# Kernel tuning notes

Hardware: AMD Instinct MI355X
Metric: run time of the kernel (lower is better)

The kernel has to match this reference:

```python
import jax, jax.numpy as jnp
import numpy as np

NUM_ITERATIONS = 3

def squash(t, axis=-1):
    sq = jnp.clip(jnp.sum(t * t, axis=axis, keepdims=True), 1e-8, 1e4)
    norm = jnp.sqrt(sq)
    scale = sq / (1.0 + sq)
    return scale * (t / (norm + 1e-8))

def setup_inputs() -> dict:
    key = jax.random.key(0)
    k1, k2 = jax.random.split(key)
    B, N_in, N_out, D_in, D_out = 128, 1152, 10, 8, 16
    u = jax.random.normal(k1, (B, N_in, D_in), dtype=jnp.float32)
    W = jax.random.normal(k2, (N_in, N_out, D_out, D_in), dtype=jnp.float32) * 0.005
    return {"u": u, "W": W}

def reference(u, W):
    # u: [B, N_in, D_in]; W: [N_in, N_out, D_out, D_in]
    # u_hat: [B, N_in, N_out, D_out]
    u_hat = jnp.einsum('iodk,bik->biod', W, u)
    u_hat = jnp.clip(u_hat, -10.0, 10.0)
    B, N_in, N_out, _ = u_hat.shape
    b = jnp.zeros((B, N_in, N_out), dtype=u_hat.dtype)
    v = None
    for it in range(NUM_ITERATIONS):
        c = jax.nn.softmax(b, axis=2)                      # [B, N_in, N_out]
        s = jnp.einsum('bio,biod->bod', c, u_hat)          # [B, N_out, D_out]
        v = squash(s, axis=-1)                             # [B, N_out, D_out]
        if it < NUM_ITERATIONS - 1:
            agreement = jnp.einsum('biod,bod->bio', u_hat, v)
            b = b + jnp.clip(agreement, -10.0, 10.0)
    return v
```

## Files before the change

### kernel.cpp

```cpp
#include <hip/hip_runtime.h>
#include <cstddef>

#define NB    128
#define NIN   1152
#define NOUT  10
#define DOUT  16
#define OD    160
#define NSEG  36
#define SEGI  32
#define PGRID (NB / 2 * NSEG)

typedef __attribute__((ext_vector_type(4))) unsigned int u32x4;

#if __has_builtin(__builtin_amdgcn_fdot2_f32_bf16)
#define HAS_DOT2 1
typedef __attribute__((ext_vector_type(2))) __bf16 bf16x2;
__device__ __forceinline__ float dot2bf(unsigned w, unsigned uu, float c) {
    return __builtin_amdgcn_fdot2_f32_bf16(
        __builtin_bit_cast(bf16x2, w), __builtin_bit_cast(bf16x2, uu), c, false);
}
#else
#define HAS_DOT2 0
#endif

__device__ __forceinline__ unsigned short f2bf(float x) {
    union { float f; unsigned u; } v; v.f = x;
    const unsigned r = v.u + 0x7fffu + ((v.u >> 16) & 1u);
    return (unsigned short)(r >> 16);
}
__device__ __forceinline__ unsigned pack2(float a, float b) {
    return (unsigned)f2bf(a) | ((unsigned)f2bf(b) << 16);
}
__device__ __forceinline__ float lo2f(unsigned w) {
    union { unsigned u; float f; } v; v.u = w << 16; return v.f;
}
__device__ __forceinline__ float hi2f(unsigned w) {
    union { unsigned u; float f; } v; v.u = w & 0xffff0000u; return v.f;
}

template<int CTRL>
__device__ __forceinline__ float dpp_f(float x) {
    return __int_as_float(__builtin_amdgcn_update_dpp(
        0, __float_as_int(x), CTRL, 0xF, 0xF, true));
}
__device__ __forceinline__ float row16_sum(float x) {
    x += dpp_f<0xB1>(x);
    x += dpp_f<0x4E>(x);
    x += dpp_f<0x124>(x);
    x += dpp_f<0x128>(x);
    return x;
}

__global__ __launch_bounds__(256)
void kprep(const float* __restrict__ W, unsigned* __restrict__ Wb)
{
    const int t = blockIdx.x * 256 + threadIdx.x;
    const float4 a = *reinterpret_cast<const float4*>(W + (size_t)t * 8);
    const float4 c = *reinterpret_cast<const float4*>(W + (size_t)t * 8 + 4);
    u32x4 o;
    o[0] = pack2(a.x, a.y); o[1] = pack2(a.z, a.w);
    o[2] = pack2(c.x, c.y); o[3] = pack2(c.z, c.w);
    *reinterpret_cast<u32x4*>(Wb + (size_t)t * 4) = o;
}

template<int PASS>
__global__ __launch_bounds__(256)
void kpass(const float* __restrict__ u, const unsigned* __restrict__ Wb,
           const float* __restrict__ p1, const float* __restrict__ p2,
           float* __restrict__ pout)
{
    __shared__ unsigned u_lds[2][SEGI * 4];
    __shared__ float red[2][16][176];
    __shared__ float sv1[2][OD], sv2[2][OD], vb[2][OD];

    const int tid   = threadIdx.x;
    const int ip    = tid >> 4;
    const int dl    = tid & 15;
    const int seg   = blockIdx.x >> 6;
    const int bpair = blockIdx.x & 63;
    const int b0    = bpair * 2;

    if (tid < 128) {
        const int bb = tid >> 6;
        const int t2 = tid & 63;
        const float4 a = *reinterpret_cast<const float4*>(
            u + ((size_t)(b0 + bb) * NIN + seg * SEGI) * 8 + (size_t)t2 * 4);
        u_lds[bb][t2 * 2]     = pack2(a.x, a.y);
        u_lds[bb][t2 * 2 + 1] = pack2(a.z, a.w);
    }

    if constexpr (PASS >= 2) {
        for (int t = tid; t < 2 * OD; t += 256) {
            const int bb = t / OD;
            const int od = t - bb * OD;
            float s = 0.0f;
            #pragma unroll
            for (int sg = 0; sg < NSEG; ++sg)
                s += p1[((size_t)(b0 + bb) * NSEG + sg) * OD + od];
            sv1[bb][od] = s;
            if constexpr (PASS == 3) {
                float s2 = 0.0f;
                #pragma unroll
                for (int sg = 0; sg < NSEG; ++sg)
                    s2 += p2[((size_t)(b0 + bb) * NSEG + sg) * OD + od];
                sv2[bb][od] = s2;
            }
        }
    }
    __syncthreads();
    if constexpr (PASS >= 2) {
        for (int t = tid; t < 2 * OD; t += 256) {
            const int bb = t / OD;
            const int od = t - bb * OD;
            const int o  = od >> 4;
            float ssq = 0.0f;
            #pragma unroll
            for (int dd = 0; dd < DOUT; ++dd) {
                const float x = sv1[bb][o * DOUT + dd];
                ssq += x * x;
            }
            ssq = fminf(1e4f, fmaxf(1e-8f, ssq));
            float v = (ssq / (1.0f + ssq)) * sv1[bb][od] / (sqrtf(ssq) + 1e-8f);
            if constexpr (PASS == 3) {
                float sq2 = 0.0f;
                #pragma unroll
                for (int dd = 0; dd < DOUT; ++dd) {
                    const float x = sv2[bb][o * DOUT + dd];
                    sq2 += x * x;
                }
                sq2 = fminf(1e4f, fmaxf(1e-8f, sq2));
                v += (sq2 / (1.0f + sq2)) * sv2[bb][od] / (sqrtf(sq2) + 1e-8f);
            }
            vb[bb][od] = v;
        }
        __syncthreads();
    }

    float vf0[NOUT], vf1[NOUT];
    if constexpr (PASS >= 2) {
        #pragma unroll
        for (int o = 0; o < NOUT; ++o) {
            vf0[o] = vb[0][o * DOUT + dl];
            vf1[o] = vb[1][o * DOUT + dl];
        }
    }
    if constexpr (PASS == 1) __syncthreads();

    float acc0[NOUT], acc1[NOUT];
    #pragma unroll
    for (int o = 0; o < NOUT; ++o) { acc0[o] = 0.0f; acc1[o] = 0.0f; }

    for (int t = 0; t < 2; ++t) {
        const int i_loc = t * 16 + ip;
        const size_t i = (size_t)seg * SEGI + i_loc;

        const u32x4 uw0 = *reinterpret_cast<const u32x4*>(&u_lds[0][i_loc * 4]);
        const u32x4 uw1 = *reinterpret_cast<const u32x4*>(&u_lds[1][i_loc * 4]);
#if !HAS_DOT2
        float ur0[8], ur1[8];
        #pragma unroll
        for (int kp = 0; kp < 4; ++kp) {
            ur0[2 * kp] = lo2f(uw0[kp]); ur0[2 * kp + 1] = hi2f(uw0[kp]);
            ur1[2 * kp] = lo2f(uw1[kp]); ur1[2 * kp + 1] = hi2f(uw1[kp]);
        }
#endif

        float uh0[NOUT], uh1[NOUT];
        #pragma unroll
        for (int o = 0; o < NOUT; ++o) {
            const u32x4 wv = *reinterpret_cast<const u32x4*>(
                Wb + ((i * NOUT + o) * DOUT + dl) * 4);
#if HAS_DOT2
            uh0[o] = dot2bf(wv[0], uw0[0], dot2bf(wv[1], uw0[1],
                     dot2bf(wv[2], uw0[2], dot2bf(wv[3], uw0[3], 0.0f))));
            uh1[o] = dot2bf(wv[0], uw1[0], dot2bf(wv[1], uw1[1],
                     dot2bf(wv[2], uw1[2], dot2bf(wv[3], uw1[3], 0.0f))));
#else
            uh0[o] = lo2f(wv[0]) * ur0[0] + hi2f(wv[0]) * ur0[1]
                   + lo2f(wv[1]) * ur0[2] + hi2f(wv[1]) * ur0[3]
                   + lo2f(wv[2]) * ur0[4] + hi2f(wv[2]) * ur0[5]
                   + lo2f(wv[3]) * ur0[6] + hi2f(wv[3]) * ur0[7];
            uh1[o] = lo2f(wv[0]) * ur1[0] + hi2f(wv[0]) * ur1[1]
                   + lo2f(wv[1]) * ur1[2] + hi2f(wv[1]) * ur1[3]
                   + lo2f(wv[2]) * ur1[4] + hi2f(wv[2]) * ur1[5]
                   + lo2f(wv[3]) * ur1[6] + hi2f(wv[3]) * ur1[7];
#endif
        }

        if constexpr (PASS == 1) {
            #pragma unroll
            for (int o = 0; o < NOUT; ++o) {
                acc0[o] += uh0[o];
                acc1[o] += uh1[o];
            }
        } else {
            float cw0[NOUT], cw1[NOUT];
            float ssum0 = 0.0f, ssum1 = 0.0f;
            #pragma unroll
            for (int o = 0; o < NOUT; ++o) {
                const float e0 = __expf(row16_sum(uh0[o] * vf0[o]));
                const float e1 = __expf(row16_sum(uh1[o] * vf1[o]));
                cw0[o] = e0; ssum0 += e0;
                cw1[o] = e1; ssum1 += e1;
            }
            const float inv0 = 1.0f / ssum0;
            const float inv1 = 1.0f / ssum1;
            #pragma unroll
            for (int o = 0; o < NOUT; ++o) {
                acc0[o] += (cw0[o] * inv0) * uh0[o];
                acc1[o] += (cw1[o] * inv1) * uh1[o];
            }
        }
    }

    #pragma unroll
    for (int o = 0; o < NOUT; ++o) {
        red[0][ip][o * DOUT + dl] = acc0[o];
        red[1][ip][o * DOUT + dl] = acc1[o];
    }
    __syncthreads();
    for (int t = tid; t < 2 * OD; t += 256) {
        const int bb = t / OD;
        const int od = t - bb * OD;
        float r = 0.0f;
        #pragma unroll
        for (int k = 0; k < 16; ++k)
            r += red[bb][k][od];
        if constexpr (PASS == 1) r *= 0.1f;
        pout[((size_t)(b0 + bb) * NSEG + seg) * OD + od] = r;
    }
}

__global__ __launch_bounds__(256)
void kout(const float* __restrict__ p3, float* __restrict__ out)
{
    const int idx = blockIdx.x * 256 + threadIdx.x;
    const int b   = idx / OD;
    const int od  = idx - b * OD;
    float s = 0.0f;
    #pragma unroll
    for (int sg = 0; sg < NSEG; ++sg)
        s += p3[((size_t)b * NSEG + sg) * OD + od];

    const float sq0 = row16_sum(s * s);
    const float sq  = fminf(1e4f, fmaxf(1e-8f, sq0));
    out[idx] = (sq / (1.0f + sq)) * s / (sqrtf(sq) + 1e-8f);
}

extern "C" void kernel_launch(void* const* d_in, const int* in_sizes, int n_in,
                              void* d_out, int out_size, void* d_ws, size_t ws_size,
                              hipStream_t stream)
{
    const float* u = (const float*)d_in[0];
    const float* W = (const float*)d_in[1];
    float* out = (float*)d_out;

    unsigned* Wb = (unsigned*)d_ws;
    float* p1 = (float*)(Wb + (size_t)NIN * NOUT * DOUT * 4);
    float* p2 = p1 + (size_t)NB * NSEG * OD;
    float* p3 = p2 + (size_t)NB * NSEG * OD;

    kprep<<<720, 256, 0, stream>>>(W, Wb);
    kpass<1><<<PGRID, 256, 0, stream>>>(u, Wb, nullptr, nullptr, p1);
    kpass<2><<<PGRID, 256, 0, stream>>>(u, Wb, p1, nullptr, p2);
    kpass<3><<<PGRID, 256, 0, stream>>>(u, Wb, p1, p2, p3);
    kout<<<NB * OD / 256, 256, 0, stream>>>(p3, out);
}
```

Measured before the change: 65.39 us.

## Compute squashed capsule outputs once per iteration in separate small kernels

Previously every kpass block re-reduced the 36 segment partials and re-ran squash for its batch pair, so each of the 36 segment blocks per batch repeated the same work. Now a small kv kernel reduces the partials and applies squash once per iteration, writing v to workspace, and kpass just loads the precomputed v values. This removes redundant global reads and two LDS sync phases from the main pass, at the cost of two extra kernel launches and their serialization.

```diff
diff --git a/kernel.cpp b/kernel.cpp
--- a/kernel.cpp
+++ b/kernel.cpp
@@ -66,12 +66,11 @@
 template<int PASS>
 __global__ __launch_bounds__(256)
 void kpass(const float* __restrict__ u, const unsigned* __restrict__ Wb,
-           const float* __restrict__ p1, const float* __restrict__ p2,
+           const float* __restrict__ vA, const float* __restrict__ vB,
            float* __restrict__ pout)
 {
     __shared__ unsigned u_lds[2][SEGI * 4];
     __shared__ float red[2][16][176];
-    __shared__ float sv1[2][OD], sv2[2][OD], vb[2][OD];
 
     const int tid   = threadIdx.x;
     const int ip    = tid >> 4;
@@ -89,62 +88,21 @@
         u_lds[bb][t2 * 2 + 1] = pack2(a.z, a.w);
     }
 
-    if constexpr (PASS >= 2) {
-        for (int t = tid; t < 2 * OD; t += 256) {
-            const int bb = t / OD;
-            const int od = t - bb * OD;
-            float s = 0.0f;
-            #pragma unroll
-            for (int sg = 0; sg < NSEG; ++sg)
-                s += p1[((size_t)(b0 + bb) * NSEG + sg) * OD + od];
-            sv1[bb][od] = s;
-            if constexpr (PASS == 3) {
-                float s2 = 0.0f;
-                #pragma unroll
-                for (int sg = 0; sg < NSEG; ++sg)
-                    s2 += p2[((size_t)(b0 + bb) * NSEG + sg) * OD + od];
-                sv2[bb][od] = s2;
-            }
-        }
-    }
-    __syncthreads();
-    if constexpr (PASS >= 2) {
-        for (int t = tid; t < 2 * OD; t += 256) {
-            const int bb = t / OD;
-            const int od = t - bb * OD;
-            const int o  = od >> 4;
-            float ssq = 0.0f;
-            #pragma unroll
-            for (int dd = 0; dd < DOUT; ++dd) {
-                const float x = sv1[bb][o * DOUT + dd];
-                ssq += x * x;
-            }
-            ssq = fminf(1e4f, fmaxf(1e-8f, ssq));
-            float v = (ssq / (1.0f + ssq)) * sv1[bb][od] / (sqrtf(ssq) + 1e-8f);
-            if constexpr (PASS == 3) {
-                float sq2 = 0.0f;
-                #pragma unroll
-                for (int dd = 0; dd < DOUT; ++dd) {
-                    const float x = sv2[bb][o * DOUT + dd];
-                    sq2 += x * x;
-                }
-                sq2 = fminf(1e4f, fmaxf(1e-8f, sq2));
-                v += (sq2 / (1.0f + sq2)) * sv2[bb][od] / (sqrtf(sq2) + 1e-8f);
-            }
-            vb[bb][od] = v;
-        }
-        __syncthreads();
-    }
-
     float vf0[NOUT], vf1[NOUT];
     if constexpr (PASS >= 2) {
         #pragma unroll
         for (int o = 0; o < NOUT; ++o) {
-            vf0[o] = vb[0][o * DOUT + dl];
-            vf1[o] = vb[1][o * DOUT + dl];
-        }
-    }
-    if constexpr (PASS == 1) __syncthreads();
+            float a0 = vA[(size_t)b0 * OD + o * DOUT + dl];
+            float a1 = vA[((size_t)b0 + 1) * OD + o * DOUT + dl];
+            if constexpr (PASS == 3) {
+                a0 += vB[(size_t)b0 * OD + o * DOUT + dl];
+                a1 += vB[((size_t)b0 + 1) * OD + o * DOUT + dl];
+            }
+            vf0[o] = a0;
+            vf1[o] = a1;
+        }
+    }
+    __syncthreads();
 
     float acc0[NOUT], acc1[NOUT];
     #pragma unroll
@@ -232,7 +190,7 @@
 }
 
 __global__ __launch_bounds__(256)
-void kout(const float* __restrict__ p3, float* __restrict__ out)
+void kv(const float* __restrict__ p, float* __restrict__ vout)
 {
     const int idx = blockIdx.x * 256 + threadIdx.x;
     const int b   = idx / OD;
@@ -240,11 +198,11 @@
     float s = 0.0f;
     #pragma unroll
     for (int sg = 0; sg < NSEG; ++sg)
-        s += p3[((size_t)b * NSEG + sg) * OD + od];
+        s += p[((size_t)b * NSEG + sg) * OD + od];
 
     const float sq0 = row16_sum(s * s);
     const float sq  = fminf(1e4f, fmaxf(1e-8f, sq0));
-    out[idx] = (sq / (1.0f + sq)) * s / (sqrtf(sq) + 1e-8f);
+    vout[idx] = (sq / (1.0f + sq)) * s / (sqrtf(sq) + 1e-8f);
 }
 
 extern "C" void kernel_launch(void* const* d_in, const int* in_sizes, int n_in,
@@ -259,10 +217,14 @@
     float* p1 = (float*)(Wb + (size_t)NIN * NOUT * DOUT * 4);
     float* p2 = p1 + (size_t)NB * NSEG * OD;
     float* p3 = p2 + (size_t)NB * NSEG * OD;
+    float* v1 = p3 + (size_t)NB * NSEG * OD;
+    float* v2 = v1 + NB * OD;
 
     kprep<<<720, 256, 0, stream>>>(W, Wb);
     kpass<1><<<PGRID, 256, 0, stream>>>(u, Wb, nullptr, nullptr, p1);
-    kpass<2><<<PGRID, 256, 0, stream>>>(u, Wb, p1, nullptr, p2);
-    kpass<3><<<PGRID, 256, 0, stream>>>(u, Wb, p1, p2, p3);
-    kout<<<NB * OD / 256, 256, 0, stream>>>(p3, out);
-}
+    kv<<<NB * OD / 256, 256, 0, stream>>>(p1, v1);
+    kpass<2><<<PGRID, 256, 0, stream>>>(u, Wb, v1, nullptr, p2);
+    kv<<<NB * OD / 256, 256, 0, stream>>>(p2, v2);
+    kpass<3><<<PGRID, 256, 0, stream>>>(u, Wb, v1, v2, p3);
+    kv<<<NB * OD / 256, 256, 0, stream>>>(p3, out);
+}
```

Measured after the change: 59.65 us (median of 2 runs). -8.8%, faster.
